# Kernel tuning notes

Measured on AMD Instinct MI355X. Metric: run time of the kernel, lower is better.

## Reference

```python
import jax, jax.numpy as jnp
import numpy as np

N_NODES = 100000
N_EDGES = 800000
D_MODEL = 128
N_HEAD = 8
LN_EPS = 1e-6


def setup_inputs() -> dict:
    key = jax.random.key(0)
    ks = jax.random.split(key, 6)
    embeds = jax.random.normal(ks[0], (N_NODES, D_MODEL), dtype=jnp.float32)
    # xavier_uniform bound for square [d, d] matrix: sqrt(6 / (d + d))
    bound = float(np.sqrt(6.0 / (D_MODEL + D_MODEL)))
    qW = jax.random.uniform(ks[1], (D_MODEL, D_MODEL), minval=-bound, maxval=bound, dtype=jnp.float32)
    kW = jax.random.uniform(ks[2], (D_MODEL, D_MODEL), minval=-bound, maxval=bound, dtype=jnp.float32)
    vW = jax.random.uniform(ks[3], (D_MODEL, D_MODEL), minval=-bound, maxval=bound, dtype=jnp.float32)
    ln_gamma = jnp.ones((D_MODEL,), dtype=jnp.float32)
    ln_beta = jnp.zeros((D_MODEL,), dtype=jnp.float32)
    edge_index = jax.random.randint(ks[4], (2, N_EDGES), 0, N_NODES, dtype=jnp.int64)
    return {"embeds": embeds, "qW": qW, "kW": kW, "vW": vW,
            "ln_gamma": ln_gamma, "ln_beta": ln_beta, "edge_index": edge_index}


def reference(embeds, qW, kW, vW, ln_gamma, ln_beta, edge_index):
    rows = edge_index[0]  # destination (softmax segment) indices, [E]
    cols = edge_index[1]  # source indices, [E]
    n_nodes, d_model = embeds.shape
    n_edges = rows.shape[0]
    head = N_HEAD
    d_head = d_model // head

    row_e = embeds[rows]                      # [E, d]
    col_e = embeds[cols]                      # [E, d]
    q = (row_e @ qW).reshape(n_edges, head, d_head)
    k = (col_e @ kW).reshape(n_edges, head, d_head)
    v = (col_e @ vW).reshape(n_edges, head, d_head)

    att = jnp.einsum('ehd,ehd->eh', q, k)     # [E, h]
    att = jnp.clip(att, -10.0, 10.0)
    exp_att = jnp.exp(att)

    # segment-softmax normalization over destination node
    att_norm = jax.ops.segment_sum(exp_att, rows, num_segments=n_nodes)  # [N, h]
    att = exp_att / (att_norm[rows] + 1e-8)   # [E, h]

    res_e = (att[:, :, None] * v).reshape(n_edges, d_model)              # [E, d]
    res = jax.ops.segment_sum(res_e, rows, num_segments=n_nodes)         # [N, d]
    res = res + embeds

    # LayerNorm(eps=1e-6) over last dim
    mean = jnp.mean(res, axis=-1, keepdims=True)
    var = jnp.mean((res - mean) ** 2, axis=-1, keepdims=True)
    out = (res - mean) * jax.lax.rsqrt(var + LN_EPS) * ln_gamma + ln_beta
    return out
```

## Files before the change

kernel.cpp:

```cpp
#include <hip/hip_runtime.h>
#include <hip/hip_bf16.h>

#define N_NODES 100000
#define N_EDGES 800000
#define D 128
#define NH 8
#define NB ((N_NODES + 255) / 256)

typedef __hip_bfloat16 bf16;
typedef __bf16 bf16x8 __attribute__((ext_vector_type(8)));
typedef float  f32x4  __attribute__((ext_vector_type(4)));

__device__ __forceinline__ unsigned short f2bu(float x) {
    bf16 b = __float2bfloat16(x);
    return *reinterpret_cast<unsigned short*>(&b);
}
__device__ __forceinline__ float bu2f(unsigned short u) {
    return __uint_as_float(((unsigned)u) << 16);
}
__device__ __forceinline__ float bfe0(unsigned u) { return __uint_as_float(u << 16); }
__device__ __forceinline__ float bfe1(unsigned u) { return __uint_as_float(u & 0xffff0000u); }

union frag_u { unsigned short u[8]; bf16x8 v; };

__global__ __launch_bounds__(256) void wf_prep(
    const float* __restrict__ Wq, const float* __restrict__ Wk, const float* __restrict__ Wv,
    unsigned short* __restrict__ Wf)
{
    int t = blockIdx.x * 256 + threadIdx.x;
    if (t >= 3 * 32 * 64) return;
    int lane = t & 63;
    int ct   = (t >> 6) & 31;
    int mat  = t >> 11;
    const float* W = (mat == 0) ? Wq : (mat == 1) ? Wk : Wv;
    int c  = ct >> 3, tt = ct & 7;
    int n  = tt * 16 + (lane & 15);
    int kb = c * 32 + (lane >> 4) * 8;
    unsigned short* dst = Wf + (size_t)mat * 32768 + (size_t)ct * 1024 + (size_t)lane * 8;
#pragma unroll
    for (int j = 0; j < 8; ++j) {
        float w  = W[(size_t)(kb + j) * D + n];
        unsigned short hb = f2bu(w);
        float lo = w - bu2f(hb);
        dst[j]       = hb;
        dst[512 + j] = f2bu(lo);
    }
}

__global__ __launch_bounds__(256) void qkv_mfma(
    const float* __restrict__ E, const unsigned short* __restrict__ Wf,
    bf16* __restrict__ Q, bf16* __restrict__ K, bf16* __restrict__ V)
{
    __shared__ unsigned short bsh[16384];
    const int tid  = threadIdx.x;
    const int wave = tid >> 6;
    const int lane = tid & 63;
    const int r0w  = blockIdx.x * 128 + wave * 32;

    const int am = lane & 15;
    const int aq = lane >> 4;

    frag_u ahi[2][4], alo[2][4];
#pragma unroll
    for (int rt = 0; rt < 2; ++rt) {
        int row = r0w + rt * 16 + am;
        if (row >= N_NODES) row = N_NODES - 1;
        const float* erow = E + (size_t)row * D + aq * 8;
#pragma unroll
        for (int c = 0; c < 4; ++c) {
            float4 e0 = *reinterpret_cast<const float4*>(erow + c * 32);
            float4 e1 = *reinterpret_cast<const float4*>(erow + c * 32 + 4);
            float ef[8] = {e0.x, e0.y, e0.z, e0.w, e1.x, e1.y, e1.z, e1.w};
#pragma unroll
            for (int j = 0; j < 8; ++j) {
                unsigned short hb = f2bu(ef[j]);
                ahi[rt][c].u[j] = hb;
                alo[rt][c].u[j] = f2bu(ef[j] - bu2f(hb));
            }
        }
    }

    bf16* const Os[3] = {Q, K, V};

#pragma unroll
    for (int mat = 0; mat < 3; ++mat) {
        f32x4 acc[8][2];
#pragma unroll
        for (int t = 0; t < 8; ++t)
#pragma unroll
            for (int rt = 0; rt < 2; ++rt)
                acc[t][rt] = (f32x4){0.f, 0.f, 0.f, 0.f};

        const unsigned short* wm = Wf + (size_t)mat * 32768;

#pragma unroll
        for (int half = 0; half < 2; ++half) {
            __syncthreads();
            const uint4* src = reinterpret_cast<const uint4*>(wm + half * 16384);
            uint4* dstv = reinterpret_cast<uint4*>(bsh);
#pragma unroll
            for (int k = 0; k < 8; ++k)
                dstv[k * 256 + tid] = src[k * 256 + tid];
            __syncthreads();

#pragma unroll
            for (int t = 0; t < 8; ++t) {
#pragma unroll
                for (int cc = 0; cc < 2; ++cc) {
                    const unsigned short* bp = bsh + (cc * 8 + t) * 1024 + lane * 8;
                    bf16x8 bhi = *reinterpret_cast<const bf16x8*>(bp);
                    bf16x8 blo = *reinterpret_cast<const bf16x8*>(bp + 512);
                    const int c = half * 2 + cc;
#pragma unroll
                    for (int rt = 0; rt < 2; ++rt) {
                        acc[t][rt] = __builtin_amdgcn_mfma_f32_16x16x32_bf16(alo[rt][c].v, bhi, acc[t][rt], 0, 0, 0);
                        acc[t][rt] = __builtin_amdgcn_mfma_f32_16x16x32_bf16(ahi[rt][c].v, blo, acc[t][rt], 0, 0, 0);
                        acc[t][rt] = __builtin_amdgcn_mfma_f32_16x16x32_bf16(ahi[rt][c].v, bhi, acc[t][rt], 0, 0, 0);
                    }
                }
            }
        }
        __syncthreads();

        unsigned short* ob = bsh + wave * 2176;
#pragma unroll
        for (int rt = 0; rt < 2; ++rt) {
#pragma unroll
            for (int t = 0; t < 8; ++t)
#pragma unroll
                for (int r = 0; r < 4; ++r)
                    ob[(aq * 4 + r) * 136 + t * 16 + am] = f2bu(acc[t][rt][r]);
            const int row = lane >> 2, c4 = lane & 3;
            int grow = r0w + rt * 16 + row;
            if (grow < N_NODES) {
                const uint4* srcb = reinterpret_cast<const uint4*>(ob + row * 136 + c4 * 32);
                uint4 d0 = srcb[0], d1 = srcb[1], d2 = srcb[2], d3 = srcb[3];
                uint4* dst = reinterpret_cast<uint4*>(Os[mat] + (size_t)grow * D + c4 * 32);
                dst[0] = d0; dst[1] = d1; dst[2] = d2; dst[3] = d3;
            }
        }
    }
}

__global__ __launch_bounds__(256) void hist_kernel(
    const int* __restrict__ rows, int* __restrict__ counts)
{
    int e = blockIdx.x * 256 + threadIdx.x;
    if (e < N_EDGES) atomicAdd(&counts[rows[e]], 1);
}

__global__ __launch_bounds__(256) void scan_block(
    const int* __restrict__ counts, int* __restrict__ scanned, int* __restrict__ block_sums)
{
    __shared__ int s[256];
    int tid = threadIdx.x;
    int i = blockIdx.x * 256 + tid;
    int v = (i < N_NODES) ? counts[i] : 0;
    s[tid] = v;
    __syncthreads();
#pragma unroll
    for (int off = 1; off < 256; off <<= 1) {
        int t = (tid >= off) ? s[tid - off] : 0;
        __syncthreads();
        s[tid] += t;
        __syncthreads();
    }
    if (i < N_NODES) scanned[i] = s[tid] - v;
    if (tid == 255) block_sums[blockIdx.x] = s[255];
}

__global__ __launch_bounds__(512) void scan_tops(int* __restrict__ block_sums)
{
    __shared__ int s[512];
    int tid = threadIdx.x;
    int v = (tid < NB) ? block_sums[tid] : 0;
    s[tid] = v;
    __syncthreads();
#pragma unroll
    for (int off = 1; off < 512; off <<= 1) {
        int t = (tid >= off) ? s[tid - off] : 0;
        __syncthreads();
        s[tid] += t;
        __syncthreads();
    }
    if (tid < NB) block_sums[tid] = s[tid] - v;
}

__global__ __launch_bounds__(256) void scan_add(
    int* __restrict__ scanned, const int* __restrict__ block_sums, int* __restrict__ cursor)
{
    int i = blockIdx.x * 256 + threadIdx.x;
    if (i < N_NODES) {
        int o = scanned[i] + block_sums[blockIdx.x];
        scanned[i] = o;
        cursor[i]  = o;
    }
}

__global__ __launch_bounds__(256) void scatter_kernel(
    const int* __restrict__ rows, const int* __restrict__ cols,
    int* __restrict__ cursor, int* __restrict__ csr_cols)
{
    int e = blockIdx.x * 256 + threadIdx.x;
    if (e < N_EDGES) {
        int pos = atomicAdd(&cursor[rows[e]], 1);
        csr_cols[pos] = cols[e];
    }
}

__global__ __launch_bounds__(256) void fused_node(
    const bf16* __restrict__ Qb, const bf16* __restrict__ Kb, const bf16* __restrict__ Vb,
    const int* __restrict__ offsets, const int* __restrict__ counts,
    const int* __restrict__ csr_cols,
    const float* __restrict__ emb,
    const float* __restrict__ gamma, const float* __restrict__ beta,
    float* __restrict__ out)
{
    int n = blockIdx.x * 4 + (threadIdx.x >> 6);
    int lane = threadIdx.x & 63;
    if (n >= N_NODES) return;

    unsigned qu = *reinterpret_cast<const unsigned*>(Qb + (size_t)n * D + lane * 2);
    float q0 = bfe0(qu), q1 = bfe1(qu);

    int start = offsets[n];
    int cnt   = counts[n];

    const bf16* kbase = Kb + lane * 2;
    const bf16* vbase = Vb + lane * 2;

    float acc0 = 0.f, acc1 = 0.f, nrm = 0.f;
    for (int base = 0; base < cnt; base += 64) {
        int m = cnt - base; if (m > 64) m = 64;
        int myc = (base + lane < cnt) ? csr_cols[start + base + lane] : 0;
        int j = 0;
        for (; j + 1 < m; j += 2) {
            int c0 = __shfl(myc, j, 64);
            int c1 = __shfl(myc, j + 1, 64);
            unsigned ku0 = *reinterpret_cast<const unsigned*>(kbase + (size_t)c0 * D);
            unsigned vu0 = *reinterpret_cast<const unsigned*>(vbase + (size_t)c0 * D);
            unsigned ku1 = *reinterpret_cast<const unsigned*>(kbase + (size_t)c1 * D);
            unsigned vu1 = *reinterpret_cast<const unsigned*>(vbase + (size_t)c1 * D);
            float p0 = q0 * bfe0(ku0) + q1 * bfe1(ku0);
            float p1 = q0 * bfe0(ku1) + q1 * bfe1(ku1);
            p0 += __shfl_xor(p0, 1, 64);
            p1 += __shfl_xor(p1, 1, 64);
            p0 += __shfl_xor(p0, 2, 64);
            p1 += __shfl_xor(p1, 2, 64);
            p0 += __shfl_xor(p0, 4, 64);
            p1 += __shfl_xor(p1, 4, 64);
            float s0 = __expf(fminf(fmaxf(p0, -10.f), 10.f));
            float s1 = __expf(fminf(fmaxf(p1, -10.f), 10.f));
            nrm  += s0 + s1;
            acc0 += s0 * bfe0(vu0) + s1 * bfe0(vu1);
            acc1 += s0 * bfe1(vu0) + s1 * bfe1(vu1);
        }
        if (j < m) {
            int c0 = __shfl(myc, j, 64);
            unsigned ku0 = *reinterpret_cast<const unsigned*>(kbase + (size_t)c0 * D);
            unsigned vu0 = *reinterpret_cast<const unsigned*>(vbase + (size_t)c0 * D);
            float p0 = q0 * bfe0(ku0) + q1 * bfe1(ku0);
            p0 += __shfl_xor(p0, 1, 64);
            p0 += __shfl_xor(p0, 2, 64);
            p0 += __shfl_xor(p0, 4, 64);
            float s0 = __expf(fminf(fmaxf(p0, -10.f), 10.f));
            nrm  += s0;
            acc0 += s0 * bfe0(vu0);
            acc1 += s0 * bfe1(vu0);
        }
    }

    float w = 1.f / (nrm + 1e-8f);
    float2 e2 = *reinterpret_cast<const float2*>(emb + (size_t)n * D + lane * 2);
    float x0 = acc0 * w + e2.x;
    float x1 = acc1 * w + e2.y;

    float ssum = x0 + x1;
#pragma unroll
    for (int off = 32; off; off >>= 1) ssum += __shfl_xor(ssum, off, 64);
    float mean = ssum * (1.0f / 128.0f);
    float d0 = x0 - mean, d1 = x1 - mean;
    float var = d0 * d0 + d1 * d1;
#pragma unroll
    for (int off = 32; off; off >>= 1) var += __shfl_xor(var, off, 64);
    float rs = rsqrtf(var * (1.0f / 128.0f) + 1e-6f);

    float2 g2 = *reinterpret_cast<const float2*>(gamma + lane * 2);
    float2 b2 = *reinterpret_cast<const float2*>(beta + lane * 2);
    float2 o2 = make_float2(d0 * rs * g2.x + b2.x, d1 * rs * g2.y + b2.y);
    *reinterpret_cast<float2*>(out + (size_t)n * D + lane * 2) = o2;
}

extern "C" void kernel_launch(void* const* d_in, const int* in_sizes, int n_in,
                              void* d_out, int out_size, void* d_ws, size_t ws_size,
                              hipStream_t stream)
{
    const float* emb   = (const float*)d_in[0];
    const float* qW    = (const float*)d_in[1];
    const float* kW    = (const float*)d_in[2];
    const float* vW    = (const float*)d_in[3];
    const float* gamma = (const float*)d_in[4];
    const float* beta  = (const float*)d_in[5];
    const int*   eidx  = (const int*)d_in[6];
    const int*   rows  = eidx;
    const int*   cols  = eidx + N_EDGES;
    float* out = (float*)d_out;

    const size_t ND = (size_t)N_NODES * D;
    bf16* Qb = (bf16*)d_ws;
    bf16* Kb = Qb + ND;
    bf16* Vb = Kb + ND;
    int* counts     = (int*)(Vb + ND);
    int* offsets    = counts + N_NODES;
    int* cursor     = offsets + N_NODES;
    int* block_sums = cursor + N_NODES;
    int* csr_cols   = block_sums + 512;
    unsigned short* Wf = (unsigned short*)(csr_cols + N_EDGES);

    hipMemsetAsync(counts, 0, (size_t)N_NODES * sizeof(int), stream);

    wf_prep<<<24, 256, 0, stream>>>(qW, kW, vW, Wf);
    qkv_mfma<<<(N_NODES + 127) / 128, 256, 0, stream>>>(emb, Wf, Qb, Kb, Vb);

    hist_kernel<<<(N_EDGES + 255) / 256, 256, 0, stream>>>(rows, counts);
    scan_block<<<NB, 256, 0, stream>>>(counts, offsets, block_sums);
    scan_tops<<<1, 512, 0, stream>>>(block_sums);
    scan_add<<<NB, 256, 0, stream>>>(offsets, block_sums, cursor);
    scatter_kernel<<<(N_EDGES + 255) / 256, 256, 0, stream>>>(rows, cols, cursor, csr_cols);

    fused_node<<<(N_NODES + 3) / 4, 256, 0, stream>>>(
        Qb, Kb, Vb, offsets, counts, csr_cols, emb, gamma, beta, out);
}
```

Baseline: 314.9 us.

## Interleave K/V rows, fuse histogram into QKV kernel, use DPP reductions

Stores K and V interleaved per node so each lane fetches both with one 8-byte gather per neighbour. It folds the counts reset into the weight prep kernel and the edge histogram into the QKV MFMA kernel, removing a memset and a launch. The attention loop uses DPP-based 8-lane reductions, exp2 with a pre-scaled query, and 4-way unrolling to raise memory-level parallelism. The trade-offs are atomics contending with the GEMM work and slightly different rounding in the exponent.

```diff
diff --git a/kernel.cpp b/kernel.cpp
--- a/kernel.cpp
+++ b/kernel.cpp
@@ -23,33 +23,48 @@
 
 union frag_u { unsigned short u[8]; bf16x8 v; };
 
-__global__ __launch_bounds__(256) void wf_prep(
+template<int CTRL>
+__device__ __forceinline__ float dpp_add(float x) {
+    int y = __builtin_amdgcn_mov_dpp(__float_as_int(x), CTRL, 0xf, 0xf, true);
+    return x + __int_as_float(y);
+}
+__device__ __forceinline__ float red8(float x) {
+    x = dpp_add<0xB1>(x);
+    x = dpp_add<0x4E>(x);
+    x = dpp_add<0x141>(x);
+    return x;
+}
+
+__global__ __launch_bounds__(256) void prep_kernel(
     const float* __restrict__ Wq, const float* __restrict__ Wk, const float* __restrict__ Wv,
-    unsigned short* __restrict__ Wf)
+    unsigned short* __restrict__ Wf, int* __restrict__ counts)
 {
     int t = blockIdx.x * 256 + threadIdx.x;
-    if (t >= 3 * 32 * 64) return;
-    int lane = t & 63;
-    int ct   = (t >> 6) & 31;
-    int mat  = t >> 11;
-    const float* W = (mat == 0) ? Wq : (mat == 1) ? Wk : Wv;
-    int c  = ct >> 3, tt = ct & 7;
-    int n  = tt * 16 + (lane & 15);
-    int kb = c * 32 + (lane >> 4) * 8;
-    unsigned short* dst = Wf + (size_t)mat * 32768 + (size_t)ct * 1024 + (size_t)lane * 8;
-#pragma unroll
-    for (int j = 0; j < 8; ++j) {
-        float w  = W[(size_t)(kb + j) * D + n];
-        unsigned short hb = f2bu(w);
-        float lo = w - bu2f(hb);
-        dst[j]       = hb;
-        dst[512 + j] = f2bu(lo);
+    if (t < N_NODES) counts[t] = 0;
+    if (t < 3 * 32 * 64) {
+        int lane = t & 63;
+        int ct   = (t >> 6) & 31;
+        int mat  = t >> 11;
+        const float* W = (mat == 0) ? Wq : (mat == 1) ? Wk : Wv;
+        int c  = ct >> 3, tt = ct & 7;
+        int n  = tt * 16 + (lane & 15);
+        int kb = c * 32 + (lane >> 4) * 8;
+        unsigned short* dst = Wf + (size_t)mat * 32768 + (size_t)ct * 1024 + (size_t)lane * 8;
+#pragma unroll
+        for (int j = 0; j < 8; ++j) {
+            float w  = W[(size_t)(kb + j) * D + n];
+            unsigned short hb = f2bu(w);
+            float lo = w - bu2f(hb);
+            dst[j]       = hb;
+            dst[512 + j] = f2bu(lo);
+        }
     }
 }
 
 __global__ __launch_bounds__(256) void qkv_mfma(
     const float* __restrict__ E, const unsigned short* __restrict__ Wf,
-    bf16* __restrict__ Q, bf16* __restrict__ K, bf16* __restrict__ V)
+    bf16* __restrict__ Q, char* __restrict__ KVb,
+    const int* __restrict__ rows, int* __restrict__ counts)
 {
     __shared__ unsigned short bsh[16384];
     const int tid  = threadIdx.x;
@@ -57,6 +72,17 @@
     const int lane = tid & 63;
     const int r0w  = blockIdx.x * 128 + wave * 32;
 
+    {
+        int e0 = (blockIdx.x * 256 + tid) * 4;
+        if (e0 < N_EDGES) {
+            int4 r4 = *reinterpret_cast<const int4*>(rows + e0);
+            atomicAdd(&counts[r4.x], 1);
+            atomicAdd(&counts[r4.y], 1);
+            atomicAdd(&counts[r4.z], 1);
+            atomicAdd(&counts[r4.w], 1);
+        }
+    }
+
     const int am = lane & 15;
     const int aq = lane >> 4;
 
@@ -79,8 +105,6 @@
             }
         }
     }
-
-    bf16* const Os[3] = {Q, K, V};
 
 #pragma unroll
     for (int mat = 0; mat < 3; ++mat) {
@@ -134,19 +158,24 @@
             int grow = r0w + rt * 16 + row;
             if (grow < N_NODES) {
                 const uint4* srcb = reinterpret_cast<const uint4*>(ob + row * 136 + c4 * 32);
-                uint4 d0 = srcb[0], d1 = srcb[1], d2 = srcb[2], d3 = srcb[3];
-                uint4* dst = reinterpret_cast<uint4*>(Os[mat] + (size_t)grow * D + c4 * 32);
-                dst[0] = d0; dst[1] = d1; dst[2] = d2; dst[3] = d3;
+                if (mat == 0) {
+                    uint4 d0 = srcb[0], d1 = srcb[1], d2 = srcb[2], d3 = srcb[3];
+                    uint4* dst = reinterpret_cast<uint4*>(Q + (size_t)grow * D + c4 * 32);
+                    dst[0] = d0; dst[1] = d1; dst[2] = d2; dst[3] = d3;
+                } else {
+                    char* dstc = KVb + ((size_t)grow << 9) + (c4 << 7) + ((mat == 2) ? 4 : 0);
+#pragma unroll
+                    for (int i = 0; i < 4; ++i) {
+                        uint4 dd = srcb[i];
+                        *reinterpret_cast<unsigned*>(dstc + i * 32 + 0)  = dd.x;
+                        *reinterpret_cast<unsigned*>(dstc + i * 32 + 8)  = dd.y;
+                        *reinterpret_cast<unsigned*>(dstc + i * 32 + 16) = dd.z;
+                        *reinterpret_cast<unsigned*>(dstc + i * 32 + 24) = dd.w;
+                    }
+                }
             }
         }
     }
-}
-
-__global__ __launch_bounds__(256) void hist_kernel(
-    const int* __restrict__ rows, int* __restrict__ counts)
-{
-    int e = blockIdx.x * 256 + threadIdx.x;
-    if (e < N_EDGES) atomicAdd(&counts[rows[e]], 1);
 }
 
 __global__ __launch_bounds__(256) void scan_block(
@@ -209,7 +238,7 @@
 }
 
 __global__ __launch_bounds__(256) void fused_node(
-    const bf16* __restrict__ Qb, const bf16* __restrict__ Kb, const bf16* __restrict__ Vb,
+    const bf16* __restrict__ Qb, const char* __restrict__ KVb,
     const int* __restrict__ offsets, const int* __restrict__ counts,
     const int* __restrict__ csr_cols,
     const float* __restrict__ emb,
@@ -218,55 +247,54 @@
 {
     int n = blockIdx.x * 4 + (threadIdx.x >> 6);
     int lane = threadIdx.x & 63;
-    if (n >= N_NODES) return;
+
+    const float L2E   = 1.44269504f;
+    const float CLIP2 = 14.4269504f;
 
     unsigned qu = *reinterpret_cast<const unsigned*>(Qb + (size_t)n * D + lane * 2);
-    float q0 = bfe0(qu), q1 = bfe1(qu);
+    float q0 = bfe0(qu) * L2E, q1 = bfe1(qu) * L2E;
 
     int start = offsets[n];
     int cnt   = counts[n];
-
-    const bf16* kbase = Kb + lane * 2;
-    const bf16* vbase = Vb + lane * 2;
+    unsigned lane8 = (unsigned)(lane << 3);
 
     float acc0 = 0.f, acc1 = 0.f, nrm = 0.f;
     for (int base = 0; base < cnt; base += 64) {
         int m = cnt - base; if (m > 64) m = 64;
-        int myc = (base + lane < cnt) ? csr_cols[start + base + lane] : 0;
+        int moff = (base + lane < cnt) ? (csr_cols[start + base + lane] << 9) : 0;
         int j = 0;
-        for (; j + 1 < m; j += 2) {
-            int c0 = __shfl(myc, j, 64);
-            int c1 = __shfl(myc, j + 1, 64);
-            unsigned ku0 = *reinterpret_cast<const unsigned*>(kbase + (size_t)c0 * D);
-            unsigned vu0 = *reinterpret_cast<const unsigned*>(vbase + (size_t)c0 * D);
-            unsigned ku1 = *reinterpret_cast<const unsigned*>(kbase + (size_t)c1 * D);
-            unsigned vu1 = *reinterpret_cast<const unsigned*>(vbase + (size_t)c1 * D);
-            float p0 = q0 * bfe0(ku0) + q1 * bfe1(ku0);
-            float p1 = q0 * bfe0(ku1) + q1 * bfe1(ku1);
-            p0 += __shfl_xor(p0, 1, 64);
-            p1 += __shfl_xor(p1, 1, 64);
-            p0 += __shfl_xor(p0, 2, 64);
-            p1 += __shfl_xor(p1, 2, 64);
-            p0 += __shfl_xor(p0, 4, 64);
-            p1 += __shfl_xor(p1, 4, 64);
-            float s0 = __expf(fminf(fmaxf(p0, -10.f), 10.f));
-            float s1 = __expf(fminf(fmaxf(p1, -10.f), 10.f));
-            nrm  += s0 + s1;
-            acc0 += s0 * bfe0(vu0) + s1 * bfe0(vu1);
-            acc1 += s0 * bfe1(vu0) + s1 * bfe1(vu1);
-        }
-        if (j < m) {
-            int c0 = __shfl(myc, j, 64);
-            unsigned ku0 = *reinterpret_cast<const unsigned*>(kbase + (size_t)c0 * D);
-            unsigned vu0 = *reinterpret_cast<const unsigned*>(vbase + (size_t)c0 * D);
-            float p0 = q0 * bfe0(ku0) + q1 * bfe1(ku0);
-            p0 += __shfl_xor(p0, 1, 64);
-            p0 += __shfl_xor(p0, 2, 64);
-            p0 += __shfl_xor(p0, 4, 64);
-            float s0 = __expf(fminf(fmaxf(p0, -10.f), 10.f));
+        for (; j + 3 < m; j += 4) {
+            int o0 = __shfl(moff, j,     64);
+            int o1 = __shfl(moff, j + 1, 64);
+            int o2 = __shfl(moff, j + 2, 64);
+            int o3 = __shfl(moff, j + 3, 64);
+            uint2 kv0 = *reinterpret_cast<const uint2*>(KVb + ((unsigned)o0 | lane8));
+            uint2 kv1 = *reinterpret_cast<const uint2*>(KVb + ((unsigned)o1 | lane8));
+            uint2 kv2 = *reinterpret_cast<const uint2*>(KVb + ((unsigned)o2 | lane8));
+            uint2 kv3 = *reinterpret_cast<const uint2*>(KVb + ((unsigned)o3 | lane8));
+            float p0 = q0 * bfe0(kv0.x) + q1 * bfe1(kv0.x);
+            float p1 = q0 * bfe0(kv1.x) + q1 * bfe1(kv1.x);
+            float p2 = q0 * bfe0(kv2.x) + q1 * bfe1(kv2.x);
+            float p3 = q0 * bfe0(kv3.x) + q1 * bfe1(kv3.x);
+            p0 = red8(p0); p1 = red8(p1); p2 = red8(p2); p3 = red8(p3);
+            float s0 = __builtin_amdgcn_exp2f(fminf(fmaxf(p0, -CLIP2), CLIP2));
+            float s1 = __builtin_amdgcn_exp2f(fminf(fmaxf(p1, -CLIP2), CLIP2));
+            float s2 = __builtin_amdgcn_exp2f(fminf(fmaxf(p2, -CLIP2), CLIP2));
+            float s3 = __builtin_amdgcn_exp2f(fminf(fmaxf(p3, -CLIP2), CLIP2));
+            nrm  += (s0 + s1) + (s2 + s3);
+            acc0 += s0 * bfe0(kv0.y); acc1 += s0 * bfe1(kv0.y);
+            acc0 += s1 * bfe0(kv1.y); acc1 += s1 * bfe1(kv1.y);
+            acc0 += s2 * bfe0(kv2.y); acc1 += s2 * bfe1(kv2.y);
+            acc0 += s3 * bfe0(kv3.y); acc1 += s3 * bfe1(kv3.y);
+        }
+        for (; j < m; ++j) {
+            int o0 = __shfl(moff, j, 64);
+            uint2 kv0 = *reinterpret_cast<const uint2*>(KVb + ((unsigned)o0 | lane8));
+            float p0 = red8(q0 * bfe0(kv0.x) + q1 * bfe1(kv0.x));
+            float s0 = __builtin_amdgcn_exp2f(fminf(fmaxf(p0, -CLIP2), CLIP2));
             nrm  += s0;
-            acc0 += s0 * bfe0(vu0);
-            acc1 += s0 * bfe1(vu0);
+            acc0 += s0 * bfe0(kv0.y);
+            acc1 += s0 * bfe1(kv0.y);
         }
     }
 
@@ -307,27 +335,23 @@
     float* out = (float*)d_out;
 
     const size_t ND = (size_t)N_NODES * D;
-    bf16* Qb = (bf16*)d_ws;
-    bf16* Kb = Qb + ND;
-    bf16* Vb = Kb + ND;
-    int* counts     = (int*)(Vb + ND);
+    bf16* Qb  = (bf16*)d_ws;
+    char* KVb = (char*)(Qb + ND);
+    int* counts     = (int*)(KVb + (size_t)N_NODES * 512);
     int* offsets    = counts + N_NODES;
     int* cursor     = offsets + N_NODES;
     int* block_sums = cursor + N_NODES;
     int* csr_cols   = block_sums + 512;
     unsigned short* Wf = (unsigned short*)(csr_cols + N_EDGES);
 
-    hipMemsetAsync(counts, 0, (size_t)N_NODES * sizeof(int), stream);
-
-    wf_prep<<<24, 256, 0, stream>>>(qW, kW, vW, Wf);
-    qkv_mfma<<<(N_NODES + 127) / 128, 256, 0, stream>>>(emb, Wf, Qb, Kb, Vb);
-
-    hist_kernel<<<(N_EDGES + 255) / 256, 256, 0, stream>>>(rows, counts);
+    prep_kernel<<<NB, 256, 0, stream>>>(qW, kW, vW, Wf, counts);
+    qkv_mfma<<<(N_NODES + 127) / 128, 256, 0, stream>>>(emb, Wf, Qb, KVb, rows, counts);
+
     scan_block<<<NB, 256, 0, stream>>>(counts, offsets, block_sums);
     scan_tops<<<1, 512, 0, stream>>>(block_sums);
     scan_add<<<NB, 256, 0, stream>>>(offsets, block_sums, cursor);
     scatter_kernel<<<(N_EDGES + 255) / 256, 256, 0, stream>>>(rows, cols, cursor, csr_cols);
 
     fused_node<<<(N_NODES + 3) / 4, 256, 0, stream>>>(
-        Qb, Kb, Vb, offsets, counts, csr_cols, emb, gamma, beta, out);
-}
+        Qb, KVb, offsets, counts, csr_cols, emb, gamma, beta, out);
+}
```

New measurement: 339.6 us. 1.08x slower.
